# Kernel optimization log

Hardware: AMD Instinct MI355X
Metric: run time of the kernel (lower is better)

Reference implementation:

```python
import jax, jax.numpy as jnp
import numpy as np

E, T, D, I, G, K = 8, 1024, 1024, 5632, 128, 2  # experts, tokens, hidden, intermediate, gptq group, topk
RENORMALIZE = True


def setup_inputs() -> dict:
    key = jax.random.key(0)
    ks = jax.random.split(key, 6)
    x = jax.random.normal(ks[0], (T, D), dtype=jnp.float32)
    gating_output = jax.random.normal(ks[1], (T, E), dtype=jnp.float32)
    # int4 GPTQ nibbles stored as int32 in [0, 16)
    w1_q = jax.random.randint(ks[2], (E, D, 2 * I), 0, 16, dtype=jnp.int32)
    w2_q = jax.random.randint(ks[3], (E, I, D), 0, 16, dtype=jnp.int32)
    # per-group scales (group size G along the input/contraction dim)
    w1_scale = jax.random.uniform(ks[4], (E, D // G, 2 * I), dtype=jnp.float32) * 0.02
    w2_scale = jax.random.uniform(ks[5], (E, I // G, D), dtype=jnp.float32) * 0.02
    return {"x": x, "gating_output": gating_output, "w1_q": w1_q, "w2_q": w2_q,
            "w1_scale": w1_scale, "w2_scale": w2_scale}


def _dequant(q, scale, group_size):
    # symmetric GPTQ int4: w = (q - 8) * scale, scale broadcast over its group
    s = jnp.repeat(scale, group_size, axis=1)  # [E, Kdim, N]
    return (q.astype(scale.dtype) - 8.0) * s


def reference(x, gating_output, w1_q, w2_q, w1_scale, w2_scale):
    w1 = _dequant(w1_q, w1_scale, G)  # [E, D, 2I]
    w2 = _dequant(w2_q, w2_scale, G)  # [E, I, D]

    # top-k softmax routing (use_grouped_topk=False path)
    probs = jax.nn.softmax(gating_output, axis=-1)        # [T, E]
    topk_w, topk_i = jax.lax.top_k(probs, K)              # [T, K]
    if RENORMALIZE:
        topk_w = topk_w / jnp.sum(topk_w, axis=-1, keepdims=True)
    # dense combine weights [T, E] (zero where expert not selected)
    cw = jnp.sum(jax.nn.one_hot(topk_i, E, dtype=x.dtype) * topk_w[..., None], axis=1)

    # expert MLPs: silu(x @ Wg) * (x @ Wu) @ Wd
    h = jnp.einsum('td,edn->etn', x, w1)                  # [E, T, 2I]
    gate, up = h[..., :I], h[..., I:]
    act = jax.nn.silu(gate) * up                          # [E, T, I]
    y = jnp.einsum('eti,eid->etd', act, w2)               # [E, T, D]

    out = jnp.einsum('te,etd->td', cw, y)                 # [T, D]
    return out
```

## Files before the change

kernel.cpp:

```cpp
#include <hip/hip_runtime.h>
#include <cstdint>
#include <cstddef>

#define E_ 8
#define T_ 1024
#define D_ 1024
#define I_ 5632
#define TWO_I_ 11264
#define NPAD_MAX 2176
#define NGRP_MAX 136

#define WS_ACTF_B 65536
#define WS_XGF_B  (65536 + 24510464)
#define WS_Y_B    WS_XGF_B
#define WS_CNT   0
#define WS_BASEP 8
#define WS_ESLOT 16
#define WS_TOKW  2064
#define WS_ETOK  4112

typedef __attribute__((ext_vector_type(8))) __bf16 bf16x8;
typedef __attribute__((ext_vector_type(4))) float  f32x4;

__device__ __forceinline__ unsigned f2bf(float f) {
    unsigned u = __float_as_uint(f);
    u += 0x7fffu + ((u >> 16) & 1u);
    return u >> 16;
}
__device__ __forceinline__ unsigned pack2bf(float f0, float f1) {
    unsigned a0 = __float_as_uint(f0); a0 += 0x7fffu + ((a0 >> 16) & 1u);
    unsigned a1 = __float_as_uint(f1); a1 += 0x7fffu + ((a1 >> 16) & 1u);
    return (a0 >> 16) | (a1 & 0xffff0000u);
}

__global__ void routing_kernel(const float* __restrict__ gate,
                               int* cnt, int* basep, int* eslot,
                               float* tokw, int* etok)
{
    int t = threadIdx.x;
    if (t < E_) cnt[t] = 0;
    __syncthreads();
    float g[E_];
#pragma unroll
    for (int e = 0; e < E_; ++e) g[e] = gate[t * E_ + e];
    int i0 = 0; float p0 = g[0];
#pragma unroll
    for (int e = 1; e < E_; ++e) if (g[e] > p0) { p0 = g[e]; i0 = e; }
    int i1 = -1; float p1 = -1e30f;
#pragma unroll
    for (int e = 0; e < E_; ++e) if (e != i0 && g[e] > p1) { p1 = g[e]; i1 = e; }
    float w0 = 1.0f / (1.0f + expf(p1 - p0));
    float w1 = 1.0f - w0;
    int s0 = atomicAdd(&cnt[i0], 1);
    int s1 = atomicAdd(&cnt[i1], 1);
    etok[i0 * T_ + s0] = t;
    etok[i1 * T_ + s1] = t;
    eslot[t * 2 + 0] = i0 * T_ + s0;  tokw[t * 2 + 0] = w0;
    eslot[t * 2 + 1] = i1 * T_ + s1;  tokw[t * 2 + 1] = w1;
    __syncthreads();
    if (t == 0) {
        int r = 0;
#pragma unroll
        for (int e = 0; e < E_; ++e) { basep[e] = r; r += (cnt[e] + 15) & ~15; }
    }
}

__global__ void gather_cast_kernel(const float* __restrict__ x,
                                   const int* __restrict__ cnt,
                                   const int* __restrict__ basep,
                                   const int* __restrict__ etok,
                                   unsigned short* __restrict__ xgf)
{
    int e = blockIdx.x >> 6, g = blockIdx.x & 63;
    int n = cnt[e];
    if (g * 16 >= n) return;
    int tid = threadIdx.x;
    int row = g * 16 + (tid & 15);
    row = min(row, n - 1);
    int tok = etok[e * T_ + row];
    const float* xr = x + (size_t)tok * D_;
    unsigned short* dst = xgf + ((size_t)(basep[e] >> 4) + g) * 16384;
#pragma unroll
    for (int it = 0; it < 8; ++it) {
        int c = it * 16 + (tid >> 4);
        float4 v0 = *(const float4*)(xr + c * 8);
        float4 v1 = *(const float4*)(xr + c * 8 + 4);
        uint4 h;
        h.x = pack2bf(v0.x, v0.y); h.y = pack2bf(v0.z, v0.w);
        h.z = pack2bf(v1.x, v1.y); h.w = pack2bf(v1.z, v1.w);
        *(uint4*)(dst + c * 128 + (tid & 15) * 8) = h;
    }
}

__global__ __launch_bounds__(256, 2) void gemm1_kernel(
    const unsigned short* __restrict__ xgf, const int* __restrict__ w1q,
    const float* __restrict__ w1s, const int* __restrict__ cnt,
    const int* __restrict__ basep, unsigned short* __restrict__ actf)
{
    int cg = blockIdx.x % 176, e = blockIdx.x / 176;
    int n = cnt[e];
    if (n <= 0) return;
    int npad = (n + 15) & ~15;
    int pb = basep[e];
    int tid = threadIdx.x, lane = tid & 63, w = tid >> 6;
    int l15 = lane & 15, lq = lane >> 4;
    int colg = w & 1, mh = w >> 1;
    int jcol = cg * 32 + colg * 16 + l15;

    const char* bg0 = (const char*)(w1q + ((size_t)e * 1024 + lq * 8) * TWO_I_ + jcol);
    const char* bu0 = bg0 + (size_t)I_ * 4;

    for (int tb = 0; tb < npad; tb += 320) {
        int aoff[10];
#pragma unroll
        for (int mi = 0; mi < 10; ++mi) {
            int R = tb + mh * 160 + mi * 16;
            R = min(R, npad - 16);
            aoff[mi] = ((pb + R) >> 4) * 32768;
        }
        const char* abase = (const char*)xgf + lq * 256 + l15 * 16;
        const char* bg = bg0;
        const char* bu = bu0;

        f32x4 accg[10], accu[10];
#pragma unroll
        for (int mi = 0; mi < 10; ++mi) {
            accg[mi] = (f32x4){0.f, 0.f, 0.f, 0.f};
            accu[mi] = (f32x4){0.f, 0.f, 0.f, 0.f};
        }
        int qg[2][8], qu[2][8];
#pragma unroll
        for (int j = 0; j < 8; ++j) {
            qg[0][j] = *(const int*)(bg + (size_t)j * 45056);
            qu[0][j] = *(const int*)(bu + (size_t)j * 45056);
        }
        bg += 1441792; bu += 1441792;
        float sg = 0.f, su = 0.f, og = 0.f, ou = 0.f;

#pragma unroll 4
        for (int t = 0; t < 32; ++t) {
            const int cur = t & 1;
            if ((t & 3) == 0) {
                const float* sp = w1s + ((size_t)e * 8 + (t >> 2)) * TWO_I_ + jcol;
                sg = sp[0]; su = sp[I_];
                og = -8.f * sg; ou = -8.f * su;
            }
            const char* at = abase + t * 1024;
            bf16x8 a[10];
#pragma unroll
            for (int mi = 0; mi < 10; ++mi)
                a[mi] = *(const bf16x8*)(at + aoff[mi]);
            union { unsigned u[4]; bf16x8 v; } fg, fu;
#pragma unroll
            for (int h = 0; h < 4; ++h) {
                fg.u[h] = pack2bf((float)qg[cur][2*h] * sg + og,
                                  (float)qg[cur][2*h+1] * sg + og);
                fu.u[h] = pack2bf((float)qu[cur][2*h] * su + ou,
                                  (float)qu[cur][2*h+1] * su + ou);
            }
            if (t < 31) {
#pragma unroll
                for (int j = 0; j < 8; ++j) {
                    qg[cur ^ 1][j] = *(const int*)(bg + (size_t)j * 45056);
                    qu[cur ^ 1][j] = *(const int*)(bu + (size_t)j * 45056);
                }
                bg += 1441792; bu += 1441792;
            }
#pragma unroll
            for (int mi = 0; mi < 10; ++mi) {
                accg[mi] = __builtin_amdgcn_mfma_f32_16x16x32_bf16(a[mi], fg.v, accg[mi], 0, 0, 0);
                accu[mi] = __builtin_amdgcn_mfma_f32_16x16x32_bf16(a[mi], fu.v, accu[mi], 0, 0, 0);
            }
        }
#pragma unroll
        for (int mi = 0; mi < 10; ++mi) {
#pragma unroll
            for (int r = 0; r < 4; ++r) {
                int ml = mh * 160 + mi * 16 + lq * 4 + r;
                int m = tb + ml;
                if (m < npad) {
                    float gv = accg[mi][r], uv = accu[mi][r];
                    float av = gv / (1.f + __expf(-gv)) * uv;
                    int prow = pb + m;
                    size_t o = (size_t)(prow >> 4) * 90112 + (jcol >> 3) * 128
                             + (prow & 15) * 8 + (jcol & 7);
                    actf[o] = (unsigned short)f2bf(av);
                }
            }
        }
    }
}

__global__ __launch_bounds__(256, 2) void gemm2_kernel(
    const unsigned short* __restrict__ actf, const int* __restrict__ w2q,
    const float* __restrict__ w2s, const int* __restrict__ cnt,
    const int* __restrict__ basep, float* __restrict__ y)
{
    int bid = blockIdx.x;
    int seg = bid & 3, dt = (bid >> 2) & 15, e = bid >> 6;
    int n = cnt[e];
    if (n <= 0) return;
    int npad = (n + 15) & ~15;
    int pb = basep[e];
    int tid = threadIdx.x, lane = tid & 63, w = tid >> 6;
    int l15 = lane & 15, lq = lane >> 4;
    int colg = w & 1, mh = w >> 1;
    int dcol = dt * 64 + colg * 32 + l15;

    const char* b00 = (const char*)(w2q + ((size_t)e * 5632 + seg * 1408 + lq * 8) * 1024 + dcol);
    float* yseg = y + (size_t)seg * NPAD_MAX * 1024;

    for (int tb = 0; tb < npad; tb += 320) {
        int aoff[10];
#pragma unroll
        for (int mi = 0; mi < 10; ++mi) {
            int R = tb + mh * 160 + mi * 16;
            R = min(R, npad - 16);
            aoff[mi] = ((pb + R) >> 4) * 180224;
        }
        const char* abase = (const char*)actf + seg * 45056 + lq * 256 + l15 * 16;
        const char* b0 = b00;

        f32x4 acc0[10], acc1[10];
#pragma unroll
        for (int mi = 0; mi < 10; ++mi) {
            acc0[mi] = (f32x4){0.f, 0.f, 0.f, 0.f};
            acc1[mi] = (f32x4){0.f, 0.f, 0.f, 0.f};
        }
        int q0[2][8], q1[2][8];
#pragma unroll
        for (int j = 0; j < 8; ++j) {
            q0[0][j] = *(const int*)(b0 + (size_t)j * 4096);
            q1[0][j] = *(const int*)(b0 + 64 + (size_t)j * 4096);
        }
        b0 += 131072;
        float s0 = 0.f, s1 = 0.f, o0 = 0.f, o1 = 0.f;

#pragma unroll 4
        for (int t = 0; t < 44; ++t) {
            const int cur = t & 1;
            if ((t & 3) == 0) {
                const float* sp = w2s + ((size_t)e * 44 + seg * 11 + (t >> 2)) * 1024 + dcol;
                s0 = sp[0]; s1 = sp[16];
                o0 = -8.f * s0; o1 = -8.f * s1;
            }
            const char* at = abase + t * 1024;
            bf16x8 a[10];
#pragma unroll
            for (int mi = 0; mi < 10; ++mi)
                a[mi] = *(const bf16x8*)(at + aoff[mi]);
            union { unsigned u[4]; bf16x8 v; } f0, f1;
#pragma unroll
            for (int h = 0; h < 4; ++h) {
                f0.u[h] = pack2bf((float)q0[cur][2*h] * s0 + o0,
                                  (float)q0[cur][2*h+1] * s0 + o0);
                f1.u[h] = pack2bf((float)q1[cur][2*h] * s1 + o1,
                                  (float)q1[cur][2*h+1] * s1 + o1);
            }
            if (t < 43) {
#pragma unroll
                for (int j = 0; j < 8; ++j) {
                    q0[cur ^ 1][j] = *(const int*)(b0 + (size_t)j * 4096);
                    q1[cur ^ 1][j] = *(const int*)(b0 + 64 + (size_t)j * 4096);
                }
                b0 += 131072;
            }
#pragma unroll
            for (int mi = 0; mi < 10; ++mi) {
                acc0[mi] = __builtin_amdgcn_mfma_f32_16x16x32_bf16(a[mi], f0.v, acc0[mi], 0, 0, 0);
                acc1[mi] = __builtin_amdgcn_mfma_f32_16x16x32_bf16(a[mi], f1.v, acc1[mi], 0, 0, 0);
            }
        }
#pragma unroll
        for (int mi = 0; mi < 10; ++mi) {
#pragma unroll
            for (int r = 0; r < 4; ++r) {
                int m = tb + mh * 160 + mi * 16 + lq * 4 + r;
                if (m < n) {
                    float* yr = yseg + (size_t)(pb + m) * 1024;
                    yr[dcol]      = acc0[mi][r];
                    yr[dcol + 16] = acc1[mi][r];
                }
            }
        }
    }
}

__global__ void combine_kernel(const float* __restrict__ y,
                               const int* __restrict__ eslot,
                               const float* __restrict__ tokw,
                               const int* __restrict__ basep,
                               float* __restrict__ out)
{
    int idx = blockIdx.x * blockDim.x + threadIdx.x;
    int t  = idx >> 8;
    int dc = idx & 255;
    int es0 = eslot[t * 2 + 0], es1 = eslot[t * 2 + 1];
    float w0 = tokw[t * 2 + 0], w1 = tokw[t * 2 + 1];
    int p0 = basep[es0 >> 10] + (es0 & 1023);
    int p1 = basep[es1 >> 10] + (es1 & 1023);
    const float4* y4 = (const float4*)y;
    float4 o = (float4){0.f, 0.f, 0.f, 0.f};
#pragma unroll
    for (int seg = 0; seg < 4; ++seg) {
        float4 a = y4[((size_t)seg * NPAD_MAX + p0) * 256 + dc];
        float4 b = y4[((size_t)seg * NPAD_MAX + p1) * 256 + dc];
        o.x += w0 * a.x + w1 * b.x;
        o.y += w0 * a.y + w1 * b.y;
        o.z += w0 * a.z + w1 * b.z;
        o.w += w0 * a.w + w1 * b.w;
    }
    ((float4*)out)[idx] = o;
}

extern "C" void kernel_launch(void* const* d_in, const int* in_sizes, int n_in,
                              void* d_out, int out_size, void* d_ws, size_t ws_size,
                              hipStream_t stream)
{
    const float* x    = (const float*)d_in[0];
    const float* gate = (const float*)d_in[1];
    const int*   w1q  = (const int*)d_in[2];
    const int*   w2q  = (const int*)d_in[3];
    const float* w1s  = (const float*)d_in[4];
    const float* w2s  = (const float*)d_in[5];
    float* out = (float*)d_out;
    int*   wsi = (int*)d_ws;
    float* wsf = (float*)d_ws;

    int*   cnt   = wsi + WS_CNT;
    int*   basep = wsi + WS_BASEP;
    int*   eslot = wsi + WS_ESLOT;
    float* tokw  = wsf + WS_TOKW;
    int*   etok  = wsi + WS_ETOK;
    unsigned short* actf = (unsigned short*)((char*)d_ws + WS_ACTF_B);
    unsigned short* xgf  = (unsigned short*)((char*)d_ws + WS_XGF_B);
    float*          y    = (float*)((char*)d_ws + WS_Y_B);

    routing_kernel<<<1, 1024, 0, stream>>>(gate, cnt, basep, eslot, tokw, etok);
    gather_cast_kernel<<<E_ * 64, 256, 0, stream>>>(x, cnt, basep, etok, xgf);
    gemm1_kernel<<<E_ * 176, 256, 0, stream>>>(xgf, w1q, w1s, cnt, basep, actf);
    gemm2_kernel<<<E_ * 16 * 4, 256, 0, stream>>>(actf, w2q, w2s, cnt, basep, y);
    combine_kernel<<<(T_ * D_ / 4) / 256, 256, 0, stream>>>(y, eslot, tokw, basep, out);
}
```

Measured before the change: 845.7 us.

## Dequantize int4 weights cooperatively into double-buffered LDS in both GEMMs

In both expert GEMM kernels, the weight tile is now loaded and dequantized once per block. Each thread handles one column and one k-group and writes bf16 fragments into a double-buffered shared-memory tile. Previously every wave separately loaded and dequantized its own B fragments, so the two waves sharing columns did the same int4 global loads and conversions twice. The cost is a __syncthreads per k-step plus the LDS writes and reads, and the prefetch distance is now two k-steps.

Measured after the change: 714.0 us. -15.6%, faster.

```diff
diff --git a/kernel.cpp b/kernel.cpp
--- a/kernel.cpp
+++ b/kernel.cpp
@@ -97,6 +97,7 @@
     const float* __restrict__ w1s, const int* __restrict__ cnt,
     const int* __restrict__ basep, unsigned short* __restrict__ actf)
 {
+    __shared__ unsigned char blds[2][4096];
     int cg = blockIdx.x % 176, e = blockIdx.x / 176;
     int n = cnt[e];
     if (n <= 0) return;
@@ -107,8 +108,30 @@
     int colg = w & 1, mh = w >> 1;
     int jcol = cg * 32 + colg * 16 + l15;
 
-    const char* bg0 = (const char*)(w1q + ((size_t)e * 1024 + lq * 8) * TWO_I_ + jcol);
-    const char* bu0 = bg0 + (size_t)I_ * 4;
+    int col64 = tid & 63, kg = tid >> 6;
+    int jb = (col64 < 32) ? (cg * 32 + col64) : (I_ + cg * 32 + (col64 - 32));
+    const int*   gq  = w1q + ((size_t)e * 1024 + kg * 8) * TWO_I_ + jb;
+    const float* sqp = w1s + (size_t)e * 8 * TWO_I_ + jb;
+    unsigned swr = (unsigned)(col64 >> 4) * 1024 + (unsigned)(kg * 16 + (col64 & 15)) * 16;
+    unsigned srd = (unsigned)colg * 1024 + (unsigned)lane * 16;
+
+    int P0[8], P1[8];
+    float sc = 0.f, oc = 0.f;
+
+#define G1_ISSUE(KS, P)                                                     \
+    { _Pragma("unroll")                                                     \
+      for (int i_ = 0; i_ < 8; ++i_)                                        \
+          P[i_] = gq[(size_t)((KS) * 32 + i_) * TWO_I_]; }
+
+#define G1_DEQW(KS, P)                                                      \
+    { if (((KS) & 3) == 0) { sc = sqp[(size_t)((KS) >> 2) * TWO_I_];        \
+                             oc = -8.f * sc; }                              \
+      uint4 fr_;                                                            \
+      fr_.x = pack2bf((float)P[0]*sc + oc, (float)P[1]*sc + oc);            \
+      fr_.y = pack2bf((float)P[2]*sc + oc, (float)P[3]*sc + oc);            \
+      fr_.z = pack2bf((float)P[4]*sc + oc, (float)P[5]*sc + oc);            \
+      fr_.w = pack2bf((float)P[6]*sc + oc, (float)P[7]*sc + oc);            \
+      *(uint4*)(&blds[(KS) & 1][swr]) = fr_; }
 
     for (int tb = 0; tb < npad; tb += 320) {
         int aoff[10];
@@ -119,8 +142,6 @@
             aoff[mi] = ((pb + R) >> 4) * 32768;
         }
         const char* abase = (const char*)xgf + lq * 256 + l15 * 16;
-        const char* bg = bg0;
-        const char* bu = bu0;
 
         f32x4 accg[10], accu[10];
 #pragma unroll
@@ -128,49 +149,36 @@
             accg[mi] = (f32x4){0.f, 0.f, 0.f, 0.f};
             accu[mi] = (f32x4){0.f, 0.f, 0.f, 0.f};
         }
-        int qg[2][8], qu[2][8];
-#pragma unroll
-        for (int j = 0; j < 8; ++j) {
-            qg[0][j] = *(const int*)(bg + (size_t)j * 45056);
-            qu[0][j] = *(const int*)(bu + (size_t)j * 45056);
-        }
-        bg += 1441792; bu += 1441792;
-        float sg = 0.f, su = 0.f, og = 0.f, ou = 0.f;
-
-#pragma unroll 4
-        for (int t = 0; t < 32; ++t) {
-            const int cur = t & 1;
-            if ((t & 3) == 0) {
-                const float* sp = w1s + ((size_t)e * 8 + (t >> 2)) * TWO_I_ + jcol;
-                sg = sp[0]; su = sp[I_];
-                og = -8.f * sg; ou = -8.f * su;
-            }
-            const char* at = abase + t * 1024;
+        G1_ISSUE(0, P0);
+        G1_ISSUE(1, P1);
+        G1_DEQW(0, P0);
+        G1_ISSUE(2, P0);
+        __syncthreads();
+
+#pragma unroll 2
+        for (int ks = 0; ks < 32; ++ks) {
+            const char* at = abase + ks * 1024;
             bf16x8 a[10];
 #pragma unroll
             for (int mi = 0; mi < 10; ++mi)
                 a[mi] = *(const bf16x8*)(at + aoff[mi]);
-            union { unsigned u[4]; bf16x8 v; } fg, fu;
-#pragma unroll
-            for (int h = 0; h < 4; ++h) {
-                fg.u[h] = pack2bf((float)qg[cur][2*h] * sg + og,
-                                  (float)qg[cur][2*h+1] * sg + og);
-                fu.u[h] = pack2bf((float)qu[cur][2*h] * su + ou,
-                                  (float)qu[cur][2*h+1] * su + ou);
-            }
-            if (t < 31) {
-#pragma unroll
-                for (int j = 0; j < 8; ++j) {
-                    qg[cur ^ 1][j] = *(const int*)(bg + (size_t)j * 45056);
-                    qu[cur ^ 1][j] = *(const int*)(bu + (size_t)j * 45056);
+            bf16x8 bg = *(const bf16x8*)(&blds[ks & 1][srd]);
+            bf16x8 bu = *(const bf16x8*)(&blds[ks & 1][srd + 2048]);
+            if (ks < 31) {
+                if (ks & 1) {
+                    G1_DEQW(ks + 1, P0);
+                    if (ks < 29) { G1_ISSUE(ks + 3, P0); }
+                } else {
+                    G1_DEQW(ks + 1, P1);
+                    if (ks < 29) { G1_ISSUE(ks + 3, P1); }
                 }
-                bg += 1441792; bu += 1441792;
             }
 #pragma unroll
             for (int mi = 0; mi < 10; ++mi) {
-                accg[mi] = __builtin_amdgcn_mfma_f32_16x16x32_bf16(a[mi], fg.v, accg[mi], 0, 0, 0);
-                accu[mi] = __builtin_amdgcn_mfma_f32_16x16x32_bf16(a[mi], fu.v, accu[mi], 0, 0, 0);
-            }
+                accg[mi] = __builtin_amdgcn_mfma_f32_16x16x32_bf16(a[mi], bg, accg[mi], 0, 0, 0);
+                accu[mi] = __builtin_amdgcn_mfma_f32_16x16x32_bf16(a[mi], bu, accu[mi], 0, 0, 0);
+            }
+            __syncthreads();
         }
 #pragma unroll
         for (int mi = 0; mi < 10; ++mi) {
@@ -189,6 +197,8 @@
             }
         }
     }
+#undef G1_ISSUE
+#undef G1_DEQW
 }
 
 __global__ __launch_bounds__(256, 2) void gemm2_kernel(
@@ -196,6 +206,7 @@
     const float* __restrict__ w2s, const int* __restrict__ cnt,
     const int* __restrict__ basep, float* __restrict__ y)
 {
+    __shared__ unsigned char blds[2][4096];
     int bid = blockIdx.x;
     int seg = bid & 3, dt = (bid >> 2) & 15, e = bid >> 6;
     int n = cnt[e];
@@ -207,8 +218,30 @@
     int colg = w & 1, mh = w >> 1;
     int dcol = dt * 64 + colg * 32 + l15;
 
-    const char* b00 = (const char*)(w2q + ((size_t)e * 5632 + seg * 1408 + lq * 8) * 1024 + dcol);
-    float* yseg = y + (size_t)seg * NPAD_MAX * 1024;
+    int col64 = tid & 63, kg = tid >> 6;
+    int colb = dt * 64 + col64;
+    const int*   gq  = w2q + ((size_t)e * 5632 + seg * 1408 + kg * 8) * 1024 + colb;
+    const float* sqp = w2s + ((size_t)e * 44 + seg * 11) * 1024 + colb;
+    unsigned swr = (unsigned)(col64 >> 4) * 1024 + (unsigned)(kg * 16 + (col64 & 15)) * 16;
+    unsigned srd = (unsigned)(colg * 2) * 1024 + (unsigned)lane * 16;
+
+    int P0[8], P1[8];
+    float sc = 0.f, oc = 0.f;
+
+#define G2_ISSUE(KS, P)                                                     \
+    { _Pragma("unroll")                                                     \
+      for (int i_ = 0; i_ < 8; ++i_)                                        \
+          P[i_] = gq[(size_t)((KS) * 32 + i_) * 1024]; }
+
+#define G2_DEQW(KS, P)                                                      \
+    { if (((KS) & 3) == 0) { sc = sqp[(size_t)((KS) >> 2) * 1024];          \
+                             oc = -8.f * sc; }                              \
+      uint4 fr_;                                                            \
+      fr_.x = pack2bf((float)P[0]*sc + oc, (float)P[1]*sc + oc);            \
+      fr_.y = pack2bf((float)P[2]*sc + oc, (float)P[3]*sc + oc);            \
+      fr_.z = pack2bf((float)P[4]*sc + oc, (float)P[5]*sc + oc);            \
+      fr_.w = pack2bf((float)P[6]*sc + oc, (float)P[7]*sc + oc);            \
+      *(uint4*)(&blds[(KS) & 1][swr]) = fr_; }
 
     for (int tb = 0; tb < npad; tb += 320) {
         int aoff[10];
@@ -219,7 +252,6 @@
             aoff[mi] = ((pb + R) >> 4) * 180224;
         }
         const char* abase = (const char*)actf + seg * 45056 + lq * 256 + l15 * 16;
-        const char* b0 = b00;
 
         f32x4 acc0[10], acc1[10];
 #pragma unroll
@@ -227,49 +259,36 @@
             acc0[mi] = (f32x4){0.f, 0.f, 0.f, 0.f};
             acc1[mi] = (f32x4){0.f, 0.f, 0.f, 0.f};
         }
-        int q0[2][8], q1[2][8];
-#pragma unroll
-        for (int j = 0; j < 8; ++j) {
-            q0[0][j] = *(const int*)(b0 + (size_t)j * 4096);
-            q1[0][j] = *(const int*)(b0 + 64 + (size_t)j * 4096);
-        }
-        b0 += 131072;
-        float s0 = 0.f, s1 = 0.f, o0 = 0.f, o1 = 0.f;
-
-#pragma unroll 4
-        for (int t = 0; t < 44; ++t) {
-            const int cur = t & 1;
-            if ((t & 3) == 0) {
-                const float* sp = w2s + ((size_t)e * 44 + seg * 11 + (t >> 2)) * 1024 + dcol;
-                s0 = sp[0]; s1 = sp[16];
-                o0 = -8.f * s0; o1 = -8.f * s1;
-            }
-            const char* at = abase + t * 1024;
+        G2_ISSUE(0, P0);
+        G2_ISSUE(1, P1);
+        G2_DEQW(0, P0);
+        G2_ISSUE(2, P0);
+        __syncthreads();
+
+#pragma unroll 2
+        for (int ks = 0; ks < 44; ++ks) {
+            const char* at = abase + ks * 1024;
             bf16x8 a[10];
 #pragma unroll
             for (int mi = 0; mi < 10; ++mi)
                 a[mi] = *(const bf16x8*)(at + aoff[mi]);
-            union { unsigned u[4]; bf16x8 v; } f0, f1;
-#pragma unroll
-            for (int h = 0; h < 4; ++h) {
-                f0.u[h] = pack2bf((float)q0[cur][2*h] * s0 + o0,
-                                  (float)q0[cur][2*h+1] * s0 + o0);
-                f1.u[h] = pack2bf((float)q1[cur][2*h] * s1 + o1,
-                                  (float)q1[cur][2*h+1] * s1 + o1);
-            }
-            if (t < 43) {
-#pragma unroll
-                for (int j = 0; j < 8; ++j) {
-                    q0[cur ^ 1][j] = *(const int*)(b0 + (size_t)j * 4096);
-                    q1[cur ^ 1][j] = *(const int*)(b0 + 64 + (size_t)j * 4096);
+            bf16x8 b0 = *(const bf16x8*)(&blds[ks & 1][srd]);
+            bf16x8 b1 = *(const bf16x8*)(&blds[ks & 1][srd + 1024]);
+            if (ks < 43) {
+                if (ks & 1) {
+                    G2_DEQW(ks + 1, P0);
+                    if (ks < 41) { G2_ISSUE(ks + 3, P0); }
+                } else {
+                    G2_DEQW(ks + 1, P1);
+                    if (ks < 41) { G2_ISSUE(ks + 3, P1); }
                 }
-                b0 += 131072;
             }
 #pragma unroll
             for (int mi = 0; mi < 10; ++mi) {
-                acc0[mi] = __builtin_amdgcn_mfma_f32_16x16x32_bf16(a[mi], f0.v, acc0[mi], 0, 0, 0);
-                acc1[mi] = __builtin_amdgcn_mfma_f32_16x16x32_bf16(a[mi], f1.v, acc1[mi], 0, 0, 0);
-            }
+                acc0[mi] = __builtin_amdgcn_mfma_f32_16x16x32_bf16(a[mi], b0, acc0[mi], 0, 0, 0);
+                acc1[mi] = __builtin_amdgcn_mfma_f32_16x16x32_bf16(a[mi], b1, acc1[mi], 0, 0, 0);
+            }
+            __syncthreads();
         }
 #pragma unroll
         for (int mi = 0; mi < 10; ++mi) {
@@ -277,13 +296,15 @@
             for (int r = 0; r < 4; ++r) {
                 int m = tb + mh * 160 + mi * 16 + lq * 4 + r;
                 if (m < n) {
-                    float* yr = yseg + (size_t)(pb + m) * 1024;
+                    float* yr = y + (size_t)seg * NPAD_MAX * 1024 + (size_t)(pb + m) * 1024;
                     yr[dcol]      = acc0[mi][r];
                     yr[dcol + 16] = acc1[mi][r];
                 }
             }
         }
     }
+#undef G2_ISSUE
+#undef G2_DEQW
 }
 
 __global__ void combine_kernel(const float* __restrict__ y,
```
